# Kernel optimization log

Measured on AMD Instinct MI355X. Metric: run time of the kernel, lower is better.

The kernel has to match this reference:

```python
import jax, jax.numpy as jnp
import numpy as np

CONNECTIVITY_WEIGHT = 1.0
HOLE_WEIGHT = 0.5
SUBSAMPLE = 128  # original strides sequences longer than 128
N_TRIPLETS = 32


def _pairwise_dist(x):
    # x: [B, Tc, D] -> Euclidean distance matrix [B, Tc, Tc] (torch.cdist p=2)
    sqn = jnp.sum(x * x, axis=-1)  # [B, Tc]
    sq = sqn[:, :, None] + sqn[:, None, :] - 2.0 * jnp.einsum('bid,bjd->bij', x, x)
    sq = jnp.maximum(sq, 0.0)
    # safe sqrt: zero gradient at zero distance (matches torch.cdist behavior)
    sq_safe = jnp.where(sq > 0, sq, 1.0)
    return jnp.where(sq > 0, jnp.sqrt(sq_safe), 0.0)


def setup_inputs() -> dict:
    key = jax.random.key(0)
    k1, k2 = jax.random.split(key)
    B, T, D = 128, 2048, 512
    latent_batch = jax.random.normal(k1, (B, T, D), dtype=jnp.float32)
    connection_threshold = jnp.ones((1,), dtype=jnp.float32)
    triplet_idx = jax.random.randint(k2, (B, N_TRIPLETS, 3), 0, SUBSAMPLE, dtype=jnp.int32)
    return {
        'latent_batch': latent_batch,
        'connection_threshold': connection_threshold,
        'triplet_idx': triplet_idx,
    }


def reference(latent_batch, connection_threshold, triplet_idx):
    B, T, D = latent_batch.shape
    stride = max(T // SUBSAMPLE, 1)
    x = latent_batch[:, ::stride, :]  # [B, Tc, D], static slice
    Tc = x.shape[1]

    d = _pairwise_dist(x)  # [B, Tc, Tc]

    threshold = jnp.abs(connection_threshold[0]) + 0.1
    # sigmoid(-(d - thr)) == sigmoid(thr - d)
    p = jax.nn.sigmoid(threshold - d)
    conn_sum = jnp.sum(p, axis=(1, 2)) - jnp.trace(p, axis1=1, axis2=2)  # [B]
    denom = Tc * (Tc - 1) + 1e-8
    connectivity_loss = 1.0 - conn_sum / denom  # [B]

    # random-triplet hole loss
    b_idx = jnp.arange(B)[:, None]
    i0, i1, i2 = triplet_idx[..., 0], triplet_idx[..., 1], triplet_idx[..., 2]
    d01 = d[b_idx, i0, i1]  # [B, N_TRIPLETS]
    d02 = d[b_idx, i0, i2]
    d12 = d[b_idx, i1, i2]
    edges = jnp.stack([d01, d02, d12], axis=-1)  # [B, N_TRIPLETS, 3]
    edge_var = jnp.var(edges, axis=-1, ddof=1)  # torch.var default unbiased
    hole_loss = jnp.mean(jnp.exp(-edge_var), axis=-1)  # [B]

    avg_loss = (CONNECTIVITY_WEIGHT * jnp.mean(connectivity_loss)
                + HOLE_WEIGHT * jnp.mean(hole_loss))
    return avg_loss
```

## Files before the change

kernel.cpp:

```cpp
#include <hip/hip_runtime.h>
#include <math.h>

#define NB 128
#define TC 128
#define HALF 64
#define DD 512
#define TSTR 16
#define KT 64
#define NT (DD/KT)
#define XP 72
#define DST 132
#define NTRIP 32

typedef __attribute__((ext_vector_type(8))) short bf16x8;
typedef __attribute__((ext_vector_type(8))) unsigned short u16x8;
typedef __attribute__((ext_vector_type(4))) float f32x4;

__device__ __forceinline__ unsigned short f2bf(float f) {
  unsigned int u = __float_as_uint(f);
  return (unsigned short)((u + 0x7fffu + ((u >> 16) & 1u)) >> 16);
}

__device__ __forceinline__ u16x8 cvt8(float4 a, float4 b) {
  u16x8 w;
  w[0]=f2bf(a.x); w[1]=f2bf(a.y); w[2]=f2bf(a.z); w[3]=f2bf(a.w);
  w[4]=f2bf(b.x); w[5]=f2bf(b.y); w[6]=f2bf(b.z); w[7]=f2bf(b.w);
  return w;
}

__global__ __launch_bounds__(512, 2) void topo_half(
    const float* __restrict__ latent,
    const float* __restrict__ thr,
    const int*   __restrict__ trip,
    float* __restrict__ ws_psum,
    float* __restrict__ ws_edge)
{
  const int blk  = blockIdx.x;
  const int s    = blk >> 7;
  const int b    = blk & 127;
  const int tid  = threadIdx.x;
  const int lane = tid & 63;
  const int wid  = tid >> 6;
  const int wrow = (wid >> 2) * 32;
  const int wcol = (wid & 3) * 32;

  __shared__ __align__(16) unsigned short xt[2][TC][XP];
  __shared__ float dmat[HALF][DST];
  __shared__ float sqn[TC];
  __shared__ float wred[8];

  const float* xb = latent + (size_t)b * (2048 * 512);

  const int srow = tid >> 2;
  const int skc  = (tid & 3) * 16;
  const float* sp = xb + (size_t)srow * (TSTR * DD) + skc;

  float4 pA[4][4], pB[4][4];
#pragma unroll
  for (int t = 0; t < 4; ++t)
#pragma unroll
    for (int q = 0; q < 4; ++q)
      pA[t][q] = *reinterpret_cast<const float4*>(sp + t * KT + q * 4);
#pragma unroll
  for (int t = 0; t < 4; ++t)
#pragma unroll
    for (int q = 0; q < 4; ++q)
      pB[t][q] = *reinterpret_cast<const float4*>(sp + (t + 4) * KT + q * 4);

  float ssq = 0.f;
  u16x8 rb[16];
#pragma unroll
  for (int t = 0; t < 4; ++t) {
    rb[2 * t]     = cvt8(pA[t][0], pA[t][1]);
    rb[2 * t + 1] = cvt8(pA[t][2], pA[t][3]);
#pragma unroll
    for (int q = 0; q < 4; ++q) {
      float4 v = pA[t][q];
      ssq += v.x * v.x + v.y * v.y + v.z * v.z + v.w * v.w;
    }
  }

  f32x4 acc[2][2];
#pragma unroll
  for (int i = 0; i < 2; ++i)
#pragma unroll
    for (int j = 0; j < 2; ++j)
#pragma unroll
      for (int r = 0; r < 4; ++r) acc[i][j][r] = 0.f;

  const int r0  = s * HALF + wrow + (lane & 15);
  const int c0  = wcol + (lane & 15);
  const int kk0 = (lane >> 4) << 3;

  *reinterpret_cast<u16x8*>(&xt[0][srow][skc])     = rb[0];
  *reinterpret_cast<u16x8*>(&xt[0][srow][skc + 8]) = rb[1];
  __syncthreads();

  for (int t = 0; t < NT; ++t) {
    if (t == 3) {
#pragma unroll
      for (int u = 0; u < 4; ++u) {
        rb[8 + 2 * u] = cvt8(pB[u][0], pB[u][1]);
        rb[9 + 2 * u] = cvt8(pB[u][2], pB[u][3]);
#pragma unroll
        for (int q = 0; q < 4; ++q) {
          float4 v = pB[u][q];
          ssq += v.x * v.x + v.y * v.y + v.z * v.z + v.w * v.w;
        }
      }
    }
    if (t + 1 < NT) {
      *reinterpret_cast<u16x8*>(&xt[(t + 1) & 1][srow][skc])     = rb[2 * t + 2];
      *reinterpret_cast<u16x8*>(&xt[(t + 1) & 1][srow][skc + 8]) = rb[2 * t + 3];
    }
    const int cur = t & 1;
#pragma unroll
    for (int sub = 0; sub < 2; ++sub) {
      const int kk = sub * 32 + kk0;
      bf16x8 a0 = *reinterpret_cast<const bf16x8*>(&xt[cur][r0][kk]);
      bf16x8 a1 = *reinterpret_cast<const bf16x8*>(&xt[cur][r0 + 16][kk]);
      bf16x8 b0 = *reinterpret_cast<const bf16x8*>(&xt[cur][c0][kk]);
      bf16x8 b1 = *reinterpret_cast<const bf16x8*>(&xt[cur][c0 + 16][kk]);
      acc[0][0] = __builtin_amdgcn_mfma_f32_16x16x32_bf16(a0, b0, acc[0][0], 0, 0, 0);
      acc[0][1] = __builtin_amdgcn_mfma_f32_16x16x32_bf16(a0, b1, acc[0][1], 0, 0, 0);
      acc[1][0] = __builtin_amdgcn_mfma_f32_16x16x32_bf16(a1, b0, acc[1][0], 0, 0, 0);
      acc[1][1] = __builtin_amdgcn_mfma_f32_16x16x32_bf16(a1, b1, acc[1][1], 0, 0, 0);
    }
    __syncthreads();
  }

  ssq += __shfl_xor(ssq, 1, 64);
  ssq += __shfl_xor(ssq, 2, 64);
  if ((tid & 3) == 0) sqn[srow] = ssq;
  __syncthreads();

  const int rbase = (lane >> 4) << 2;
  const int cidx  = lane & 15;
  const float thv = fabsf(thr[0]) + 0.1f;
  float psum = 0.f;
#pragma unroll
  for (int fr = 0; fr < 2; ++fr)
#pragma unroll
    for (int fc = 0; fc < 2; ++fc)
#pragma unroll
      for (int reg = 0; reg < 4; ++reg) {
        int growL = wrow + fr * 16 + rbase + reg;
        int grow  = s * HALF + growL;
        int gcol  = wcol + fc * 16 + cidx;
        float d = 0.f;
        if (grow != gcol) {
          float g  = acc[fr][fc][reg];
          float sq = fmaxf(sqn[grow] + sqn[gcol] - 2.f * g, 0.f);
          d = sqrtf(sq);
          psum += 1.f / (1.f + __expf(d - thv));
        }
        dmat[growL][gcol] = d;
      }

#pragma unroll
  for (int off = 32; off; off >>= 1) psum += __shfl_down(psum, off, 64);
  if (lane == 0) wred[wid] = psum;
  __syncthreads();

  if (wid == 0) {
    if (lane < NTRIP) {
      const int* tp = trip + ((size_t)b * NTRIP + lane) * 3;
      const int i0 = tp[0], i1 = tp[1], i2 = tp[2];
      const size_t ebase = ((size_t)b * NTRIP + lane) * 3;
      int ps[3] = {i0, i0, i1};
      int qs[3] = {i1, i2, i2};
#pragma unroll
      for (int e = 0; e < 3; ++e) {
        int p = ps[e], q = qs[e];
        int mx = p > q ? p : q, mn = p > q ? q : p;
        if ((mx >> 6) == s)
          ws_edge[ebase + e] = (mx == mn) ? 0.f : dmat[mx - s * HALF][mn];
      }
    }
    if (lane == 0) {
      float conn = 0.f;
#pragma unroll
      for (int w = 0; w < 8; ++w) conn += wred[w];
      ws_psum[blk] = conn;
    }
  }
}

__global__ __launch_bounds__(1024) void topo_final(
    const float* __restrict__ ws_psum,
    const float* __restrict__ ws_edge,
    float* __restrict__ out)
{
  const int t    = threadIdx.x;
  const int lane = t & 63;
  const int wid  = t >> 6;

  float ps = (t < 2 * NB) ? ws_psum[t] : 0.f;
  float hs = 0.f;
#pragma unroll
  for (int k = 0; k < 4; ++k) {
    int id = t + 1024 * k;
    float e0 = ws_edge[id * 3 + 0];
    float e1 = ws_edge[id * 3 + 1];
    float e2 = ws_edge[id * 3 + 2];
    float m  = (e0 + e1 + e2) * (1.f / 3.f);
    float d0 = e0 - m, d1 = e1 - m, d2 = e2 - m;
    float v  = (d0 * d0 + d1 * d1 + d2 * d2) * 0.5f;
    hs += __expf(-v);
  }

#pragma unroll
  for (int off = 32; off; off >>= 1) {
    ps += __shfl_down(ps, off, 64);
    hs += __shfl_down(hs, off, 64);
  }
  __shared__ float rp[16], rh[16];
  if (lane == 0) { rp[wid] = ps; rh[wid] = hs; }
  __syncthreads();
  if (t == 0) {
    float Ps = 0.f, Hs = 0.f;
#pragma unroll
    for (int w = 0; w < 16; ++w) { Ps += rp[w]; Hs += rh[w]; }
    out[0] = 1.f - Ps / (16256.f * NB) + 0.5f * (Hs / (NB * NTRIP));
  }
}

extern "C" void kernel_launch(void* const* d_in, const int* in_sizes, int n_in,
                              void* d_out, int out_size, void* d_ws, size_t ws_size,
                              hipStream_t stream) {
  const float* latent = (const float*)d_in[0];
  const float* thr    = (const float*)d_in[1];
  const int*   trip   = (const int*)d_in[2];

  float* ws_psum = (float*)d_ws;
  float* ws_edge = ws_psum + 2 * NB;

  topo_half<<<2 * NB, 512, 0, stream>>>(latent, thr, trip, ws_psum, ws_edge);
  topo_final<<<1, 1024, 0, stream>>>(ws_psum, ws_edge, (float*)d_out);
}
```

Measured before the change: 18.68 us.

## Stage full swizzled bf16 tile in LDS and drop per-k-tile barriers

Each block now loads all 128 strided rows into one 128x512 bf16 LDS buffer, using wave-per-row coalesced float4 loads with an XOR swizzle. Row sums of squares are reduced with wave shuffles as rows are written. The MFMA loop then runs over all of K with no per-tile __syncthreads. To fit in LDS, the distance scratch matrix is stored as fp16, which lowers the precision of the gathered triplet edges and cuts in-flight global loads per thread compared with the old fully prefetched register pipeline.

```diff
diff --git a/kernel.cpp b/kernel.cpp
--- a/kernel.cpp
+++ b/kernel.cpp
@@ -1,4 +1,5 @@
 #include <hip/hip_runtime.h>
+#include <hip/hip_fp16.h>
 #include <math.h>
 
 #define NB 128
@@ -6,26 +7,16 @@
 #define HALF 64
 #define DD 512
 #define TSTR 16
-#define KT 64
-#define NT (DD/KT)
-#define XP 72
-#define DST 132
 #define NTRIP 32
+#define DSTH 130
 
 typedef __attribute__((ext_vector_type(8))) short bf16x8;
-typedef __attribute__((ext_vector_type(8))) unsigned short u16x8;
+typedef __attribute__((ext_vector_type(4))) unsigned short u16x4;
 typedef __attribute__((ext_vector_type(4))) float f32x4;
 
 __device__ __forceinline__ unsigned short f2bf(float f) {
   unsigned int u = __float_as_uint(f);
   return (unsigned short)((u + 0x7fffu + ((u >> 16) & 1u)) >> 16);
-}
-
-__device__ __forceinline__ u16x8 cvt8(float4 a, float4 b) {
-  u16x8 w;
-  w[0]=f2bf(a.x); w[1]=f2bf(a.y); w[2]=f2bf(a.z); w[3]=f2bf(a.w);
-  w[4]=f2bf(b.x); w[5]=f2bf(b.y); w[6]=f2bf(b.z); w[7]=f2bf(b.w);
-  return w;
 }
 
 __global__ __launch_bounds__(512, 2) void topo_half(
@@ -39,103 +30,88 @@
   const int s    = blk >> 7;
   const int b    = blk & 127;
   const int tid  = threadIdx.x;
-  const int lane = tid & 63;
+  const int l    = tid & 63;
   const int wid  = tid >> 6;
-  const int wrow = (wid >> 2) * 32;
-  const int wcol = (wid & 3) * 32;
-
-  __shared__ __align__(16) unsigned short xt[2][TC][XP];
-  __shared__ float dmat[HALF][DST];
+
+  __shared__ unsigned short xs[TC * DD];
+  __shared__ __half dmat[HALF][DSTH];
   __shared__ float sqn[TC];
   __shared__ float wred[8];
 
   const float* xb = latent + (size_t)b * (2048 * 512);
 
-  const int srow = tid >> 2;
-  const int skc  = (tid & 3) * 16;
-  const float* sp = xb + (size_t)srow * (TSTR * DD) + skc;
-
-  float4 pA[4][4], pB[4][4];
-#pragma unroll
-  for (int t = 0; t < 4; ++t)
-#pragma unroll
-    for (int q = 0; q < 4; ++q)
-      pA[t][q] = *reinterpret_cast<const float4*>(sp + t * KT + q * 4);
-#pragma unroll
-  for (int t = 0; t < 4; ++t)
-#pragma unroll
-    for (int q = 0; q < 4; ++q)
-      pB[t][q] = *reinterpret_cast<const float4*>(sp + (t + 4) * KT + q * 4);
-
-  float ssq = 0.f;
-  u16x8 rb[16];
-#pragma unroll
-  for (int t = 0; t < 4; ++t) {
-    rb[2 * t]     = cvt8(pA[t][0], pA[t][1]);
-    rb[2 * t + 1] = cvt8(pA[t][2], pA[t][3]);
-#pragma unroll
-    for (int q = 0; q < 4; ++q) {
-      float4 v = pA[t][q];
-      ssq += v.x * v.x + v.y * v.y + v.z * v.z + v.w * v.w;
+#define LOAD_GROUP(dst, base_row)                                           \
+  _Pragma("unroll") for (int k = 0; k < 4; ++k) {                           \
+    const float* rp = xb + (size_t)((base_row) + k) * (TSTR * DD) + (l << 2); \
+    dst[2 * k]     = *reinterpret_cast<const float4*>(rp);                  \
+    dst[2 * k + 1] = *reinterpret_cast<const float4*>(rp + 256);            \
+  }
+
+#define PROC_GROUP(srcv, base_row)                                          \
+  _Pragma("unroll") for (int k = 0; k < 4; ++k) {                           \
+    const int r = (base_row) + k;                                           \
+    float4 h0 = srcv[2 * k], h1 = srcv[2 * k + 1];                          \
+    u16x4 w0, w1;                                                           \
+    w0[0]=f2bf(h0.x); w0[1]=f2bf(h0.y); w0[2]=f2bf(h0.z); w0[3]=f2bf(h0.w); \
+    w1[0]=f2bf(h1.x); w1[1]=f2bf(h1.y); w1[2]=f2bf(h1.z); w1[3]=f2bf(h1.w); \
+    const int sw = (r & 7) << 3;                                            \
+    *reinterpret_cast<u16x4*>(&xs[(r * DD + (l << 2)) ^ sw])       = w0;    \
+    *reinterpret_cast<u16x4*>(&xs[(r * DD + 256 + (l << 2)) ^ sw]) = w1;    \
+    float ss = h0.x*h0.x + h0.y*h0.y + h0.z*h0.z + h0.w*h0.w                \
+             + h1.x*h1.x + h1.y*h1.y + h1.z*h1.z + h1.w*h1.w;               \
+    ss += __shfl_xor(ss, 1, 64);  ss += __shfl_xor(ss, 2, 64);              \
+    ss += __shfl_xor(ss, 4, 64);  ss += __shfl_xor(ss, 8, 64);              \
+    ss += __shfl_xor(ss, 16, 64); ss += __shfl_xor(ss, 32, 64);             \
+    if (l == 0) sqn[r] = ss;                                                \
+  }
+
+  {
+    const int rb = wid * 16;
+    float4 bufA[8], bufB[8];
+    LOAD_GROUP(bufA, rb);
+    LOAD_GROUP(bufB, rb + 4);
+    PROC_GROUP(bufA, rb);
+    LOAD_GROUP(bufA, rb + 8);
+    PROC_GROUP(bufB, rb + 4);
+    LOAD_GROUP(bufB, rb + 12);
+    PROC_GROUP(bufA, rb + 8);
+    PROC_GROUP(bufB, rb + 12);
+  }
+  __syncthreads();
+
+  const int wr = wid >> 2, wc = wid & 3;
+  const int ar0 = s * HALF + wr * 32 + (l & 15);
+  const int br0 = wc * 32 + (l & 15);
+  const int kk0 = (l >> 4) << 3;
+
+  f32x4 acc[2][2];
+#pragma unroll
+  for (int i = 0; i < 2; ++i)
+#pragma unroll
+    for (int j = 0; j < 2; ++j)
+#pragma unroll
+      for (int r = 0; r < 4; ++r) acc[i][j][r] = 0.f;
+
+  const int swA = (ar0 & 7) << 3;
+  const int swB = (br0 & 7) << 3;
+#pragma unroll
+  for (int t = 0; t < 8; ++t) {
+#pragma unroll
+    for (int sub = 0; sub < 2; ++sub) {
+      const int kc = t * 64 + sub * 32 + kk0;
+      bf16x8 A0 = *reinterpret_cast<const bf16x8*>(&xs[(ar0 * DD + kc) ^ swA]);
+      bf16x8 A1 = *reinterpret_cast<const bf16x8*>(&xs[((ar0 + 16) * DD + kc) ^ swA]);
+      bf16x8 B0 = *reinterpret_cast<const bf16x8*>(&xs[(br0 * DD + kc) ^ swB]);
+      bf16x8 B1 = *reinterpret_cast<const bf16x8*>(&xs[((br0 + 16) * DD + kc) ^ swB]);
+      acc[0][0] = __builtin_amdgcn_mfma_f32_16x16x32_bf16(A0, B0, acc[0][0], 0, 0, 0);
+      acc[0][1] = __builtin_amdgcn_mfma_f32_16x16x32_bf16(A0, B1, acc[0][1], 0, 0, 0);
+      acc[1][0] = __builtin_amdgcn_mfma_f32_16x16x32_bf16(A1, B0, acc[1][0], 0, 0, 0);
+      acc[1][1] = __builtin_amdgcn_mfma_f32_16x16x32_bf16(A1, B1, acc[1][1], 0, 0, 0);
     }
   }
 
-  f32x4 acc[2][2];
-#pragma unroll
-  for (int i = 0; i < 2; ++i)
-#pragma unroll
-    for (int j = 0; j < 2; ++j)
-#pragma unroll
-      for (int r = 0; r < 4; ++r) acc[i][j][r] = 0.f;
-
-  const int r0  = s * HALF + wrow + (lane & 15);
-  const int c0  = wcol + (lane & 15);
-  const int kk0 = (lane >> 4) << 3;
-
-  *reinterpret_cast<u16x8*>(&xt[0][srow][skc])     = rb[0];
-  *reinterpret_cast<u16x8*>(&xt[0][srow][skc + 8]) = rb[1];
-  __syncthreads();
-
-  for (int t = 0; t < NT; ++t) {
-    if (t == 3) {
-#pragma unroll
-      for (int u = 0; u < 4; ++u) {
-        rb[8 + 2 * u] = cvt8(pB[u][0], pB[u][1]);
-        rb[9 + 2 * u] = cvt8(pB[u][2], pB[u][3]);
-#pragma unroll
-        for (int q = 0; q < 4; ++q) {
-          float4 v = pB[u][q];
-          ssq += v.x * v.x + v.y * v.y + v.z * v.z + v.w * v.w;
-        }
-      }
-    }
-    if (t + 1 < NT) {
-      *reinterpret_cast<u16x8*>(&xt[(t + 1) & 1][srow][skc])     = rb[2 * t + 2];
-      *reinterpret_cast<u16x8*>(&xt[(t + 1) & 1][srow][skc + 8]) = rb[2 * t + 3];
-    }
-    const int cur = t & 1;
-#pragma unroll
-    for (int sub = 0; sub < 2; ++sub) {
-      const int kk = sub * 32 + kk0;
-      bf16x8 a0 = *reinterpret_cast<const bf16x8*>(&xt[cur][r0][kk]);
-      bf16x8 a1 = *reinterpret_cast<const bf16x8*>(&xt[cur][r0 + 16][kk]);
-      bf16x8 b0 = *reinterpret_cast<const bf16x8*>(&xt[cur][c0][kk]);
-      bf16x8 b1 = *reinterpret_cast<const bf16x8*>(&xt[cur][c0 + 16][kk]);
-      acc[0][0] = __builtin_amdgcn_mfma_f32_16x16x32_bf16(a0, b0, acc[0][0], 0, 0, 0);
-      acc[0][1] = __builtin_amdgcn_mfma_f32_16x16x32_bf16(a0, b1, acc[0][1], 0, 0, 0);
-      acc[1][0] = __builtin_amdgcn_mfma_f32_16x16x32_bf16(a1, b0, acc[1][0], 0, 0, 0);
-      acc[1][1] = __builtin_amdgcn_mfma_f32_16x16x32_bf16(a1, b1, acc[1][1], 0, 0, 0);
-    }
-    __syncthreads();
-  }
-
-  ssq += __shfl_xor(ssq, 1, 64);
-  ssq += __shfl_xor(ssq, 2, 64);
-  if ((tid & 3) == 0) sqn[srow] = ssq;
-  __syncthreads();
-
-  const int rbase = (lane >> 4) << 2;
-  const int cidx  = lane & 15;
+  const int rbase = (l >> 4) << 2;
+  const int cidx  = l & 15;
   const float thv = fabsf(thr[0]) + 0.1f;
   float psum = 0.f;
 #pragma unroll
@@ -144,9 +120,9 @@
     for (int fc = 0; fc < 2; ++fc)
 #pragma unroll
       for (int reg = 0; reg < 4; ++reg) {
-        int growL = wrow + fr * 16 + rbase + reg;
+        int growL = wr * 32 + fr * 16 + rbase + reg;
         int grow  = s * HALF + growL;
-        int gcol  = wcol + fc * 16 + cidx;
+        int gcol  = wc * 32 + fc * 16 + cidx;
         float d = 0.f;
         if (grow != gcol) {
           float g  = acc[fr][fc][reg];
@@ -154,19 +130,19 @@
           d = sqrtf(sq);
           psum += 1.f / (1.f + __expf(d - thv));
         }
-        dmat[growL][gcol] = d;
+        dmat[growL][gcol] = __float2half(d);
       }
 
 #pragma unroll
   for (int off = 32; off; off >>= 1) psum += __shfl_down(psum, off, 64);
-  if (lane == 0) wred[wid] = psum;
+  if (l == 0) wred[wid] = psum;
   __syncthreads();
 
   if (wid == 0) {
-    if (lane < NTRIP) {
-      const int* tp = trip + ((size_t)b * NTRIP + lane) * 3;
+    if (l < NTRIP) {
+      const int* tp = trip + ((size_t)b * NTRIP + l) * 3;
       const int i0 = tp[0], i1 = tp[1], i2 = tp[2];
-      const size_t ebase = ((size_t)b * NTRIP + lane) * 3;
+      const size_t ebase = ((size_t)b * NTRIP + l) * 3;
       int ps[3] = {i0, i0, i1};
       int qs[3] = {i1, i2, i2};
 #pragma unroll
@@ -174,10 +150,11 @@
         int p = ps[e], q = qs[e];
         int mx = p > q ? p : q, mn = p > q ? q : p;
         if ((mx >> 6) == s)
-          ws_edge[ebase + e] = (mx == mn) ? 0.f : dmat[mx - s * HALF][mn];
+          ws_edge[ebase + e] = (mx == mn) ? 0.f
+                             : __half2float(dmat[mx - s * HALF][mn]);
       }
     }
-    if (lane == 0) {
+    if (l == 0) {
       float conn = 0.f;
 #pragma unroll
       for (int w = 0; w < 8; ++w) conn += wred[w];
```

New measurement: 19.06 us, median of 2. +2.0%, slower.
